# Performance work log

Hardware: AMD Instinct MI355X
Metric: run time of the kernel (lower is better)

## Reference

```python
import jax, jax.numpy as jnp
import numpy as np

EMBED_DIM = 1024
PROJ_DIM = 512
NUM_HEADS = 8
HEAD_DIM = PROJ_DIM // NUM_HEADS
B, L = 2, 2048


def setup_inputs() -> dict:
    key = jax.random.key(0)
    ks = jax.random.split(key, 7)
    s = lambda d: 1.0 / np.sqrt(d)
    return {
        "x": jax.random.normal(ks[0], (B, L, EMBED_DIM), jnp.float32),
        "proj_W": jax.random.normal(ks[1], (EMBED_DIM, PROJ_DIM), jnp.float32) * s(EMBED_DIM),
        "proj_b": jax.random.normal(ks[2], (PROJ_DIM,), jnp.float32) * 0.01,
        "attn_Wq": jax.random.normal(ks[3], (PROJ_DIM, NUM_HEADS, HEAD_DIM), jnp.float32) * s(PROJ_DIM),
        "attn_Wk": jax.random.normal(ks[4], (PROJ_DIM, NUM_HEADS, HEAD_DIM), jnp.float32) * s(PROJ_DIM),
        "attn_Wv": jax.random.normal(ks[5], (PROJ_DIM, NUM_HEADS, HEAD_DIM), jnp.float32) * s(PROJ_DIM),
        "out_W": jax.random.normal(ks[6], (NUM_HEADS * HEAD_DIM, EMBED_DIM), jnp.float32) * s(NUM_HEADS * HEAD_DIM),
    }


def reference(x, proj_W, proj_b, attn_Wq, attn_Wk, attn_Wv, out_W):
    # ReLU projection: (B, L, embed_dim) -> (B, L, proj_dim)
    p = jax.nn.relu(x @ proj_W + proj_b)
    # Per-head projections: (B, L, C) x (C, H, Dh) -> (B, H, L, Dh)
    q = jnp.einsum('blc,chd->bhld', p, attn_Wq)
    k = jnp.einsum('blc,chd->bhld', p, attn_Wk)
    v = jnp.einsum('blc,chd->bhld', p, attn_Wv)
    scale = 1.0 / np.sqrt(HEAD_DIM).astype(np.float32)
    scores = jnp.einsum('bhqd,bhkd->bhqk', q, k) * scale  # (B, H, L, L)
    weights = jax.nn.softmax(scores, axis=-1)
    heads = jnp.einsum('bhqk,bhkd->bhqd', weights, v)  # (B, H, L, Dh)
    heads = heads.transpose(0, 2, 1, 3).reshape(p.shape[0], p.shape[1], NUM_HEADS * HEAD_DIM)
    return heads @ out_W  # (B, L, embed_dim)
```

## Files before the change

### kernel.cpp

```cpp
#include <hip/hip_runtime.h>
#include <math.h>

#define BATCH 2
#define SEQ 2048
#define BL (BATCH * SEQ)
#define EMBED 1024
#define PROJ 512
#define NHEADS 8
#define HDIM 64
#define QKVN (3 * PROJ)
#define KVSPLIT 2
#define KVHALF (SEQ / KVSPLIT)

typedef _Float16 half8 __attribute__((ext_vector_type(8)));
typedef float floatx4 __attribute__((ext_vector_type(4)));

__global__ __launch_bounds__(256) void trconv(const float* __restrict__ src,
                                              _Float16* __restrict__ dst,
                                              int K, int N, float scale) {
    __shared__ float tile[64][65];
    const int t  = threadIdx.x;
    const int n0 = blockIdx.x * 64;
    const int k0 = blockIdx.y * 64;
    const int tx = t & 63;
    const int ty = t >> 6;
#pragma unroll
    for (int i = 0; i < 16; ++i) {
        int k = ty * 16 + i;
        tile[k][tx] = src[(size_t)(k0 + k) * N + n0 + tx];
    }
    __syncthreads();
#pragma unroll
    for (int i = 0; i < 16; ++i) {
        int n = ty * 16 + i;
        dst[(size_t)(n0 + n) * K + k0 + tx] = (_Float16)(tile[tx][n] * scale);
    }
}

__global__ __launch_bounds__(256) void trans_v(const _Float16* __restrict__ v,
                                               _Float16* __restrict__ vt) {
    __shared__ _Float16 tile[64][72];
    const int t  = threadIdx.x;
    const int t0 = blockIdx.x * 64;
    const int h  = blockIdx.y;
    const int b  = blockIdx.z;
    {
        const int r = t >> 2, c0 = (t & 3) * 16;
        const _Float16* src = v + (size_t)(b * SEQ + t0 + r) * QKVN + h * HDIM + c0;
        *reinterpret_cast<half8*>(&tile[r][c0])     = *reinterpret_cast<const half8*>(src);
        *reinterpret_cast<half8*>(&tile[r][c0 + 8]) = *reinterpret_cast<const half8*>(src + 8);
    }
    __syncthreads();
    {
        const int c = t >> 2, k0 = (t & 3) * 16;
        half8 o1, o2;
#pragma unroll
        for (int i = 0; i < 8; ++i) { o1[i] = tile[k0 + i][c]; o2[i] = tile[k0 + 8 + i][c]; }
        _Float16* dst = vt + ((size_t)(b * NHEADS + h) * HDIM + c) * SEQ + t0 + k0;
        *reinterpret_cast<half8*>(dst)     = o1;
        *reinterpret_cast<half8*>(dst + 8) = o2;
    }
}

template <int A_F32, int BIASRELU, int C_F32>
__global__ __launch_bounds__(256) void gemm_mfma(const void* __restrict__ Ap,
                                                 const _Float16* __restrict__ Bt,
                                                 const float* __restrict__ bias,
                                                 void* __restrict__ Cp,
                                                 int M, int N, int K) {
    __shared__ _Float16 Ah[64][40];
    __shared__ _Float16 Bh[64][40];

    const int t  = threadIdx.x;
    const int w  = t >> 6;
    const int l  = t & 63;
    const int lr = l & 15;
    const int lg = l >> 4;
    const int bm = blockIdx.y * 64;
    const int bn = blockIdx.x * 64;
    const int wr = w >> 1;
    const int wc = w & 1;

    const int ar = t >> 2, ac = (t & 3) * 8;

    floatx4 acc[2][2];
#pragma unroll
    for (int i = 0; i < 2; ++i)
#pragma unroll
        for (int j = 0; j < 2; ++j) acc[i][j] = (floatx4){0.f, 0.f, 0.f, 0.f};

    float4 af0, af1;
    half8 areg, breg;

    const float* Af = (const float*)Ap;
    const _Float16* Ah16 = (const _Float16*)Ap;

    if (A_F32) {
        af0 = *reinterpret_cast<const float4*>(&Af[(size_t)(bm + ar) * K + ac]);
        af1 = *reinterpret_cast<const float4*>(&Af[(size_t)(bm + ar) * K + ac + 4]);
    } else {
        areg = *reinterpret_cast<const half8*>(&Ah16[(size_t)(bm + ar) * K + ac]);
    }
    breg = *reinterpret_cast<const half8*>(&Bt[(size_t)(bn + ar) * K + ac]);

    for (int kt = 0; kt < K; kt += 32) {
        if (A_F32) {
            half8 hcv;
            hcv[0] = (_Float16)af0.x; hcv[1] = (_Float16)af0.y;
            hcv[2] = (_Float16)af0.z; hcv[3] = (_Float16)af0.w;
            hcv[4] = (_Float16)af1.x; hcv[5] = (_Float16)af1.y;
            hcv[6] = (_Float16)af1.z; hcv[7] = (_Float16)af1.w;
            *reinterpret_cast<half8*>(&Ah[ar][ac]) = hcv;
        } else {
            *reinterpret_cast<half8*>(&Ah[ar][ac]) = areg;
        }
        *reinterpret_cast<half8*>(&Bh[ar][ac]) = breg;
        __syncthreads();

        if (kt + 32 < K) {
            if (A_F32) {
                af0 = *reinterpret_cast<const float4*>(&Af[(size_t)(bm + ar) * K + kt + 32 + ac]);
                af1 = *reinterpret_cast<const float4*>(&Af[(size_t)(bm + ar) * K + kt + 32 + ac + 4]);
            } else {
                areg = *reinterpret_cast<const half8*>(&Ah16[(size_t)(bm + ar) * K + kt + 32 + ac]);
            }
            breg = *reinterpret_cast<const half8*>(&Bt[(size_t)(bn + ar) * K + kt + 32 + ac]);
        }

        half8 afr[2], bfr[2];
#pragma unroll
        for (int mf = 0; mf < 2; ++mf)
            afr[mf] = *reinterpret_cast<const half8*>(&Ah[wr * 32 + mf * 16 + lr][lg * 8]);
#pragma unroll
        for (int nf = 0; nf < 2; ++nf)
            bfr[nf] = *reinterpret_cast<const half8*>(&Bh[wc * 32 + nf * 16 + lr][lg * 8]);
#pragma unroll
        for (int mf = 0; mf < 2; ++mf)
#pragma unroll
            for (int nf = 0; nf < 2; ++nf)
                acc[mf][nf] = __builtin_amdgcn_mfma_f32_16x16x32_f16(afr[mf], bfr[nf], acc[mf][nf], 0, 0, 0);

        __syncthreads();
    }

#pragma unroll
    for (int mf = 0; mf < 2; ++mf)
#pragma unroll
        for (int nf = 0; nf < 2; ++nf) {
            const int n = bn + wc * 32 + nf * 16 + lr;
            float bs = 0.f;
            if (BIASRELU) bs = bias[n];
#pragma unroll
            for (int r = 0; r < 4; ++r) {
                const int m = bm + wr * 32 + mf * 16 + lg * 4 + r;
                float v = acc[mf][nf][r];
                if (BIASRELU) v = fmaxf(v + bs, 0.f);
                if (C_F32)
                    ((float*)Cp)[(size_t)m * N + n] = v;
                else
                    ((_Float16*)Cp)[(size_t)m * N + n] = (_Float16)v;
            }
        }
}

__global__ __launch_bounds__(256) void attn_part(const _Float16* __restrict__ Q,
                                                 const _Float16* __restrict__ K,
                                                 const _Float16* __restrict__ Vt,
                                                 float* __restrict__ Op,
                                                 float* __restrict__ ml) {
    __shared__ _Float16 Ks[64][72];
    __shared__ _Float16 Vs[64][72];
    __shared__ _Float16 Ps[4][16][72];

    const int t  = threadIdx.x;
    const int w  = t >> 6;
    const int l  = t & 63;
    const int lr = l & 15;
    const int lg = l >> 4;

    const int qt  = blockIdx.x >> 1;
    const int kvh = blockIdx.x & 1;
    const int q0  = qt * 64;
    const int h   = blockIdx.y;
    const int b   = blockIdx.z;
    const size_t base  = (size_t)b * SEQ * QKVN + (size_t)h * HDIM;
    const size_t vbase = (size_t)(b * NHEADS + h) * HDIM * SEQ;
    const size_t poff  = (((size_t)kvh * BATCH + b) * NHEADS + h) * SEQ;

    const int kt0  = kvh * KVHALF;
    const int kend = kt0 + KVHALF;

    half8 qf[2];
#pragma unroll
    for (int s = 0; s < 2; ++s) {
        const int qrow = q0 + w * 16 + lr;
        qf[s] = *reinterpret_cast<const half8*>(
            &Q[base + (size_t)qrow * QKVN + s * 32 + lg * 8]);
    }

    floatx4 o_acc[4];
#pragma unroll
    for (int j = 0; j < 4; ++j) o_acc[j] = (floatx4){0.f, 0.f, 0.f, 0.f};

    float m_s = -1e30f;
    float l_s = 0.f;

    const int rkv = t >> 2;
    const int d0  = (t & 3) * 16;

    half8 ka0, ka1, va0, va1;
    {
        const _Float16* kp = K + base + (size_t)(kt0 + rkv) * QKVN + d0;
        ka0 = *reinterpret_cast<const half8*>(kp);
        ka1 = *reinterpret_cast<const half8*>(kp + 8);
        const _Float16* vp = Vt + vbase + (size_t)rkv * SEQ + kt0 + d0;
        va0 = *reinterpret_cast<const half8*>(vp);
        va1 = *reinterpret_cast<const half8*>(vp + 8);
    }

    for (int kt = kt0; kt < kend; kt += 64) {
        *reinterpret_cast<half8*>(&Ks[rkv][d0])     = ka0;
        *reinterpret_cast<half8*>(&Ks[rkv][d0 + 8]) = ka1;
        *reinterpret_cast<half8*>(&Vs[rkv][d0])     = va0;
        *reinterpret_cast<half8*>(&Vs[rkv][d0 + 8]) = va1;
        __syncthreads();

        if (kt + 64 < kend) {
            const _Float16* kp = K + base + (size_t)(kt + 64 + rkv) * QKVN + d0;
            ka0 = *reinterpret_cast<const half8*>(kp);
            ka1 = *reinterpret_cast<const half8*>(kp + 8);
            const _Float16* vp = Vt + vbase + (size_t)rkv * SEQ + kt + 64 + d0;
            va0 = *reinterpret_cast<const half8*>(vp);
            va1 = *reinterpret_cast<const half8*>(vp + 8);
        }

        floatx4 stv[4];
#pragma unroll
        for (int i = 0; i < 4; ++i) stv[i] = (floatx4){0.f, 0.f, 0.f, 0.f};
#pragma unroll
        for (int s = 0; s < 2; ++s)
#pragma unroll
            for (int mf = 0; mf < 4; ++mf) {
                half8 kfr = *reinterpret_cast<const half8*>(&Ks[mf * 16 + lr][s * 32 + lg * 8]);
                stv[mf] = __builtin_amdgcn_mfma_f32_16x16x32_f16(kfr, qf[s], stv[mf], 0, 0, 0);
            }

        float tm = -1e30f;
#pragma unroll
        for (int mf = 0; mf < 4; ++mf)
#pragma unroll
            for (int r = 0; r < 4; ++r) tm = fmaxf(tm, stv[mf][r]);
        tm = fmaxf(tm, __shfl_xor(tm, 16));
        tm = fmaxf(tm, __shfl_xor(tm, 32));
        float mn = fmaxf(m_s, tm);
        float fscale = exp2f(m_s - mn);
        m_s = mn;
        float sum = 0.f;
#pragma unroll
        for (int mf = 0; mf < 4; ++mf)
#pragma unroll
            for (int r = 0; r < 4; ++r) {
                float p = exp2f(stv[mf][r] - mn);
                stv[mf][r] = p;
                sum += p;
            }
        sum += __shfl_xor(sum, 16);
        sum += __shfl_xor(sum, 32);
        l_s = l_s * fscale + sum;

#pragma unroll
        for (int mf = 0; mf < 4; ++mf)
#pragma unroll
            for (int rp = 0; rp < 2; ++rp) {
                union { _Float16 hh[2]; unsigned int u; } pk;
                pk.hh[0] = (_Float16)stv[mf][2 * rp];
                pk.hh[1] = (_Float16)stv[mf][2 * rp + 1];
                *reinterpret_cast<unsigned int*>(
                    &Ps[w][lr][mf * 16 + lg * 4 + rp * 2]) = pk.u;
            }

#pragma unroll
        for (int r = 0; r < 4; ++r) {
            float f = __shfl(fscale, lg * 4 + r);
#pragma unroll
            for (int nf = 0; nf < 4; ++nf) o_acc[nf][r] *= f;
        }

#pragma unroll
        for (int s = 0; s < 2; ++s) {
            half8 pa = *reinterpret_cast<const half8*>(&Ps[w][lr][s * 32 + lg * 8]);
#pragma unroll
            for (int nf = 0; nf < 4; ++nf) {
                half8 vb = *reinterpret_cast<const half8*>(&Vs[nf * 16 + lr][s * 32 + lg * 8]);
                o_acc[nf] = __builtin_amdgcn_mfma_f32_16x16x32_f16(pa, vb, o_acc[nf], 0, 0, 0);
            }
        }

        __syncthreads();
    }

#pragma unroll
    for (int r = 0; r < 4; ++r) {
        const int qrow = q0 + w * 16 + lg * 4 + r;
#pragma unroll
        for (int nf = 0; nf < 4; ++nf)
            Op[(poff + qrow) * HDIM + nf * 16 + lr] = o_acc[nf][r];
    }
    if (lg == 0) {
        const int qrow = q0 + w * 16 + lr;
        reinterpret_cast<float2*>(ml)[poff + qrow] = make_float2(m_s, l_s);
    }
}

__global__ __launch_bounds__(256) void attn_merge(const float* __restrict__ Op,
                                                  const float* __restrict__ ml,
                                                  _Float16* __restrict__ hd) {
    const int t  = threadIdx.x;
    const int q  = blockIdx.x * 64 + (t >> 2);
    const int d0 = (t & 3) * 16;
    const int h  = blockIdx.y;
    const int b  = blockIdx.z;

    const size_t off0 = ((size_t)b * NHEADS + h) * SEQ + q;
    const size_t off1 = ((size_t)(BATCH + b) * NHEADS + h) * SEQ + q;

    float2 ml0 = reinterpret_cast<const float2*>(ml)[off0];
    float2 ml1 = reinterpret_cast<const float2*>(ml)[off1];
    float m  = fmaxf(ml0.x, ml1.x);
    float a0 = exp2f(ml0.x - m);
    float a1 = exp2f(ml1.x - m);
    float inv = 1.0f / (ml0.y * a0 + ml1.y * a1);
    a0 *= inv; a1 *= inv;

    const float* p0 = Op + off0 * HDIM + d0;
    const float* p1 = Op + off1 * HDIM + d0;
    half8 o[2];
#pragma unroll
    for (int i = 0; i < 4; ++i) {
        float4 v0 = reinterpret_cast<const float4*>(p0)[i];
        float4 v1 = reinterpret_cast<const float4*>(p1)[i];
        o[i >> 1][(i & 1) * 4 + 0] = (_Float16)(v0.x * a0 + v1.x * a1);
        o[i >> 1][(i & 1) * 4 + 1] = (_Float16)(v0.y * a0 + v1.y * a1);
        o[i >> 1][(i & 1) * 4 + 2] = (_Float16)(v0.z * a0 + v1.z * a1);
        o[i >> 1][(i & 1) * 4 + 3] = (_Float16)(v0.w * a0 + v1.w * a1);
    }
    _Float16* dst = hd + (size_t)(b * SEQ + q) * PROJ + h * HDIM + d0;
    *reinterpret_cast<half8*>(dst)     = o[0];
    *reinterpret_cast<half8*>(dst + 8) = o[1];
}

extern "C" void kernel_launch(void* const* d_in, const int* in_sizes, int n_in,
                              void* d_out, int out_size, void* d_ws, size_t ws_size,
                              hipStream_t stream) {
    const float* x  = (const float*)d_in[0];
    const float* pW = (const float*)d_in[1];
    const float* pb = (const float*)d_in[2];
    const float* Wq = (const float*)d_in[3];
    const float* Wk = (const float*)d_in[4];
    const float* Wv = (const float*)d_in[5];
    const float* oW = (const float*)d_in[6];
    float* out = (float*)d_out;

    _Float16* ws    = (_Float16*)d_ws;
    _Float16* p_h   = ws;
    _Float16* qkv   = p_h + (size_t)BL * PROJ;
    _Float16* hd    = qkv + (size_t)BL * QKVN;
    _Float16* pWt   = hd + (size_t)BL * PROJ;
    _Float16* qkvWt = pWt + (size_t)PROJ * EMBED;
    _Float16* oWt   = qkvWt + (size_t)QKVN * PROJ;
    _Float16* vtb   = oWt + (size_t)EMBED * PROJ;
    float*    Opart = (float*)(vtb + (size_t)BATCH * NHEADS * HDIM * SEQ);
    float*    mlb   = Opart + (size_t)KVSPLIT * BATCH * NHEADS * SEQ * HDIM;

    dim3 blk(256);

    trconv<<<dim3(PROJ / 64, EMBED / 64), blk, 0, stream>>>(pW, pWt, EMBED, PROJ, 1.0f);
    trconv<<<dim3(PROJ / 64, PROJ / 64), blk, 0, stream>>>(Wq, qkvWt, PROJ, PROJ, 0.125f * 1.44269504f);
    trconv<<<dim3(PROJ / 64, PROJ / 64), blk, 0, stream>>>(Wk, qkvWt + (size_t)PROJ * PROJ, PROJ, PROJ, 1.0f);
    trconv<<<dim3(PROJ / 64, PROJ / 64), blk, 0, stream>>>(Wv, qkvWt + (size_t)2 * PROJ * PROJ, PROJ, PROJ, 1.0f);
    trconv<<<dim3(EMBED / 64, PROJ / 64), blk, 0, stream>>>(oW, oWt, PROJ, EMBED, 1.0f);

    gemm_mfma<1, 1, 0><<<dim3(PROJ / 64, BL / 64), blk, 0, stream>>>(
        (const void*)x, pWt, pb, (void*)p_h, BL, PROJ, EMBED);

    gemm_mfma<0, 0, 0><<<dim3(QKVN / 64, BL / 64), blk, 0, stream>>>(
        (const void*)p_h, qkvWt, nullptr, (void*)qkv, BL, QKVN, PROJ);

    trans_v<<<dim3(SEQ / 64, NHEADS, BATCH), blk, 0, stream>>>(qkv + 2 * PROJ, vtb);

    attn_part<<<dim3((SEQ / 64) * KVSPLIT, NHEADS, BATCH), blk, 0, stream>>>(
        qkv, qkv + PROJ, vtb, Opart, mlb);
    attn_merge<<<dim3(SEQ / 64, NHEADS, BATCH), blk, 0, stream>>>(Opart, mlb, hd);

    gemm_mfma<0, 0, 1><<<dim3(EMBED / 64, BL / 64), blk, 0, stream>>>(
        (const void*)hd, oWt, nullptr, (void*)out, BL, EMBED, PROJ);
}
```

Before: 122.9 us.

## Templatize GEMM tiles, split KV four ways, lazy rescale, fp16 partials

The GEMM kernel is templated on its block tile, and the QKV and output projections use larger 128-row tiles for more operand reuse. Attention now splits the KV range four ways for more parallelism. Online softmax rescaling is skipped unless the running max grows by more than a threshold, and probabilities are packed to fp16 with cvt_pkrtz. Partial outputs are normalized and stored as fp16 to cut merge traffic, and s_setprio is raised around the MFMA sections. In exchange, the fp16 partials and lazy rescale cost some precision, and the bigger tiles launch fewer blocks.

Result: faster. 115.4 us (-6.2%).

```diff
diff --git a/kernel.cpp b/kernel.cpp
--- a/kernel.cpp
+++ b/kernel.cpp
@@ -9,10 +9,11 @@
 #define NHEADS 8
 #define HDIM 64
 #define QKVN (3 * PROJ)
-#define KVSPLIT 2
-#define KVHALF (SEQ / KVSPLIT)
+#define KVSPLIT 4
+#define KVQ (SEQ / KVSPLIT)
 
 typedef _Float16 half8 __attribute__((ext_vector_type(8)));
+typedef __fp16 fp16x2 __attribute__((ext_vector_type(2)));
 typedef float floatx4 __attribute__((ext_vector_type(4)));
 
 __global__ __launch_bounds__(256) void trconv(const float* __restrict__ src,
@@ -62,97 +63,126 @@
     }
 }
 
-template <int A_F32, int BIASRELU, int C_F32>
+template <int BM, int BN, int A_F32, int BIASRELU, int C_F32>
 __global__ __launch_bounds__(256) void gemm_mfma(const void* __restrict__ Ap,
                                                  const _Float16* __restrict__ Bt,
                                                  const float* __restrict__ bias,
                                                  void* __restrict__ Cp,
                                                  int M, int N, int K) {
-    __shared__ _Float16 Ah[64][40];
-    __shared__ _Float16 Bh[64][40];
+    __shared__ _Float16 Ah[BM][40];
+    __shared__ _Float16 Bh[BN][40];
+
+    constexpr int MF = BM / 32;
+    constexpr int NF = BN / 32;
+    constexpr int EPA = BM / 8;
+    constexpr int TPA = 32 / EPA;
+    constexpr int EPB = BN / 8;
+    constexpr int TPB = 32 / EPB;
 
     const int t  = threadIdx.x;
     const int w  = t >> 6;
     const int l  = t & 63;
     const int lr = l & 15;
     const int lg = l >> 4;
-    const int bm = blockIdx.y * 64;
-    const int bn = blockIdx.x * 64;
+    const int bm = blockIdx.y * BM;
+    const int bn = blockIdx.x * BN;
     const int wr = w >> 1;
     const int wc = w & 1;
 
-    const int ar = t >> 2, ac = (t & 3) * 8;
-
-    floatx4 acc[2][2];
-#pragma unroll
-    for (int i = 0; i < 2; ++i)
-#pragma unroll
-        for (int j = 0; j < 2; ++j) acc[i][j] = (floatx4){0.f, 0.f, 0.f, 0.f};
-
-    float4 af0, af1;
-    half8 areg, breg;
+    const int ar = t / TPA, ac = (t % TPA) * EPA;
+    const int br = t / TPB, bc = (t % TPB) * EPB;
+
+    floatx4 acc[MF][NF];
+#pragma unroll
+    for (int i = 0; i < MF; ++i)
+#pragma unroll
+        for (int j = 0; j < NF; ++j) acc[i][j] = (floatx4){0.f, 0.f, 0.f, 0.f};
+
+    float4 af[EPA / 4];
+    half8  ah[EPA / 8];
+    half8  bh[EPB / 8];
 
     const float* Af = (const float*)Ap;
     const _Float16* Ah16 = (const _Float16*)Ap;
 
     if (A_F32) {
-        af0 = *reinterpret_cast<const float4*>(&Af[(size_t)(bm + ar) * K + ac]);
-        af1 = *reinterpret_cast<const float4*>(&Af[(size_t)(bm + ar) * K + ac + 4]);
+#pragma unroll
+        for (int i = 0; i < EPA / 4; ++i)
+            af[i] = *reinterpret_cast<const float4*>(&Af[(size_t)(bm + ar) * K + ac + i * 4]);
     } else {
-        areg = *reinterpret_cast<const half8*>(&Ah16[(size_t)(bm + ar) * K + ac]);
-    }
-    breg = *reinterpret_cast<const half8*>(&Bt[(size_t)(bn + ar) * K + ac]);
+#pragma unroll
+        for (int i = 0; i < EPA / 8; ++i)
+            ah[i] = *reinterpret_cast<const half8*>(&Ah16[(size_t)(bm + ar) * K + ac + i * 8]);
+    }
+#pragma unroll
+    for (int i = 0; i < EPB / 8; ++i)
+        bh[i] = *reinterpret_cast<const half8*>(&Bt[(size_t)(bn + br) * K + bc + i * 8]);
 
     for (int kt = 0; kt < K; kt += 32) {
         if (A_F32) {
-            half8 hcv;
-            hcv[0] = (_Float16)af0.x; hcv[1] = (_Float16)af0.y;
-            hcv[2] = (_Float16)af0.z; hcv[3] = (_Float16)af0.w;
-            hcv[4] = (_Float16)af1.x; hcv[5] = (_Float16)af1.y;
-            hcv[6] = (_Float16)af1.z; hcv[7] = (_Float16)af1.w;
-            *reinterpret_cast<half8*>(&Ah[ar][ac]) = hcv;
+#pragma unroll
+            for (int i = 0; i < EPA / 8; ++i) {
+                half8 hcv;
+                float4 a0 = af[2 * i], a1 = af[2 * i + 1];
+                hcv[0] = (_Float16)a0.x; hcv[1] = (_Float16)a0.y;
+                hcv[2] = (_Float16)a0.z; hcv[3] = (_Float16)a0.w;
+                hcv[4] = (_Float16)a1.x; hcv[5] = (_Float16)a1.y;
+                hcv[6] = (_Float16)a1.z; hcv[7] = (_Float16)a1.w;
+                *reinterpret_cast<half8*>(&Ah[ar][ac + i * 8]) = hcv;
+            }
         } else {
-            *reinterpret_cast<half8*>(&Ah[ar][ac]) = areg;
-        }
-        *reinterpret_cast<half8*>(&Bh[ar][ac]) = breg;
+#pragma unroll
+            for (int i = 0; i < EPA / 8; ++i)
+                *reinterpret_cast<half8*>(&Ah[ar][ac + i * 8]) = ah[i];
+        }
+#pragma unroll
+        for (int i = 0; i < EPB / 8; ++i)
+            *reinterpret_cast<half8*>(&Bh[br][bc + i * 8]) = bh[i];
         __syncthreads();
 
         if (kt + 32 < K) {
             if (A_F32) {
-                af0 = *reinterpret_cast<const float4*>(&Af[(size_t)(bm + ar) * K + kt + 32 + ac]);
-                af1 = *reinterpret_cast<const float4*>(&Af[(size_t)(bm + ar) * K + kt + 32 + ac + 4]);
+#pragma unroll
+                for (int i = 0; i < EPA / 4; ++i)
+                    af[i] = *reinterpret_cast<const float4*>(&Af[(size_t)(bm + ar) * K + kt + 32 + ac + i * 4]);
             } else {
-                areg = *reinterpret_cast<const half8*>(&Ah16[(size_t)(bm + ar) * K + kt + 32 + ac]);
-            }
-            breg = *reinterpret_cast<const half8*>(&Bt[(size_t)(bn + ar) * K + kt + 32 + ac]);
-        }
-
-        half8 afr[2], bfr[2];
-#pragma unroll
-        for (int mf = 0; mf < 2; ++mf)
-            afr[mf] = *reinterpret_cast<const half8*>(&Ah[wr * 32 + mf * 16 + lr][lg * 8]);
-#pragma unroll
-        for (int nf = 0; nf < 2; ++nf)
-            bfr[nf] = *reinterpret_cast<const half8*>(&Bh[wc * 32 + nf * 16 + lr][lg * 8]);
-#pragma unroll
-        for (int mf = 0; mf < 2; ++mf)
-#pragma unroll
-            for (int nf = 0; nf < 2; ++nf)
+#pragma unroll
+                for (int i = 0; i < EPA / 8; ++i)
+                    ah[i] = *reinterpret_cast<const half8*>(&Ah16[(size_t)(bm + ar) * K + kt + 32 + ac + i * 8]);
+            }
+#pragma unroll
+            for (int i = 0; i < EPB / 8; ++i)
+                bh[i] = *reinterpret_cast<const half8*>(&Bt[(size_t)(bn + br) * K + kt + 32 + bc + i * 8]);
+        }
+
+        half8 afr[MF], bfr[NF];
+#pragma unroll
+        for (int mf = 0; mf < MF; ++mf)
+            afr[mf] = *reinterpret_cast<const half8*>(&Ah[wr * (BM / 2) + mf * 16 + lr][lg * 8]);
+#pragma unroll
+        for (int nf = 0; nf < NF; ++nf)
+            bfr[nf] = *reinterpret_cast<const half8*>(&Bh[wc * (BN / 2) + nf * 16 + lr][lg * 8]);
+        __builtin_amdgcn_s_setprio(1);
+#pragma unroll
+        for (int mf = 0; mf < MF; ++mf)
+#pragma unroll
+            for (int nf = 0; nf < NF; ++nf)
                 acc[mf][nf] = __builtin_amdgcn_mfma_f32_16x16x32_f16(afr[mf], bfr[nf], acc[mf][nf], 0, 0, 0);
+        __builtin_amdgcn_s_setprio(0);
 
         __syncthreads();
     }
 
 #pragma unroll
-    for (int mf = 0; mf < 2; ++mf)
-#pragma unroll
-        for (int nf = 0; nf < 2; ++nf) {
-            const int n = bn + wc * 32 + nf * 16 + lr;
+    for (int mf = 0; mf < MF; ++mf)
+#pragma unroll
+        for (int nf = 0; nf < NF; ++nf) {
+            const int n = bn + wc * (BN / 2) + nf * 16 + lr;
             float bs = 0.f;
             if (BIASRELU) bs = bias[n];
 #pragma unroll
             for (int r = 0; r < 4; ++r) {
-                const int m = bm + wr * 32 + mf * 16 + lg * 4 + r;
+                const int m = bm + wr * (BM / 2) + mf * 16 + lg * 4 + r;
                 float v = acc[mf][nf][r];
                 if (BIASRELU) v = fmaxf(v + bs, 0.f);
                 if (C_F32)
@@ -166,7 +196,7 @@
 __global__ __launch_bounds__(256) void attn_part(const _Float16* __restrict__ Q,
                                                  const _Float16* __restrict__ K,
                                                  const _Float16* __restrict__ Vt,
-                                                 float* __restrict__ Op,
+                                                 _Float16* __restrict__ Op,
                                                  float* __restrict__ ml) {
     __shared__ _Float16 Ks[64][72];
     __shared__ _Float16 Vs[64][72];
@@ -178,17 +208,17 @@
     const int lr = l & 15;
     const int lg = l >> 4;
 
-    const int qt  = blockIdx.x >> 1;
-    const int kvh = blockIdx.x & 1;
+    const int qt  = blockIdx.x >> 2;
+    const int kvs = blockIdx.x & 3;
     const int q0  = qt * 64;
     const int h   = blockIdx.y;
     const int b   = blockIdx.z;
     const size_t base  = (size_t)b * SEQ * QKVN + (size_t)h * HDIM;
     const size_t vbase = (size_t)(b * NHEADS + h) * HDIM * SEQ;
-    const size_t poff  = (((size_t)kvh * BATCH + b) * NHEADS + h) * SEQ;
-
-    const int kt0  = kvh * KVHALF;
-    const int kend = kt0 + KVHALF;
+    const size_t poff  = (((size_t)kvs * BATCH + b) * NHEADS + h) * SEQ;
+
+    const int kt0  = kvs * KVQ;
+    const int kend = kt0 + KVQ;
 
     half8 qf[2];
 #pragma unroll
@@ -237,6 +267,7 @@
         floatx4 stv[4];
 #pragma unroll
         for (int i = 0; i < 4; ++i) stv[i] = (floatx4){0.f, 0.f, 0.f, 0.f};
+        __builtin_amdgcn_s_setprio(1);
 #pragma unroll
         for (int s = 0; s < 2; ++s)
 #pragma unroll
@@ -244,6 +275,7 @@
                 half8 kfr = *reinterpret_cast<const half8*>(&Ks[mf * 16 + lr][s * 32 + lg * 8]);
                 stv[mf] = __builtin_amdgcn_mfma_f32_16x16x32_f16(kfr, qf[s], stv[mf], 0, 0, 0);
             }
+        __builtin_amdgcn_s_setprio(0);
 
         float tm = -1e30f;
 #pragma unroll
@@ -252,40 +284,40 @@
             for (int r = 0; r < 4; ++r) tm = fmaxf(tm, stv[mf][r]);
         tm = fmaxf(tm, __shfl_xor(tm, 16));
         tm = fmaxf(tm, __shfl_xor(tm, 32));
-        float mn = fmaxf(m_s, tm);
-        float fscale = exp2f(m_s - mn);
-        m_s = mn;
+        if (!__all(tm <= m_s + 8.f)) {
+            float mn = fmaxf(m_s, tm);
+            float fs = exp2f(m_s - mn);
+            m_s = mn;
+            l_s *= fs;
+#pragma unroll
+            for (int r = 0; r < 4; ++r) {
+                float f = __shfl(fs, lg * 4 + r);
+#pragma unroll
+                for (int nf = 0; nf < 4; ++nf) o_acc[nf][r] *= f;
+            }
+        }
         float sum = 0.f;
 #pragma unroll
         for (int mf = 0; mf < 4; ++mf)
 #pragma unroll
             for (int r = 0; r < 4; ++r) {
-                float p = exp2f(stv[mf][r] - mn);
+                float p = exp2f(stv[mf][r] - m_s);
                 stv[mf][r] = p;
                 sum += p;
             }
         sum += __shfl_xor(sum, 16);
         sum += __shfl_xor(sum, 32);
-        l_s = l_s * fscale + sum;
-
-#pragma unroll
-        for (int mf = 0; mf < 4; ++mf)
-#pragma unroll
-            for (int rp = 0; rp < 2; ++rp) {
-                union { _Float16 hh[2]; unsigned int u; } pk;
-                pk.hh[0] = (_Float16)stv[mf][2 * rp];
-                pk.hh[1] = (_Float16)stv[mf][2 * rp + 1];
-                *reinterpret_cast<unsigned int*>(
-                    &Ps[w][lr][mf * 16 + lg * 4 + rp * 2]) = pk.u;
-            }
-
-#pragma unroll
-        for (int r = 0; r < 4; ++r) {
-            float f = __shfl(fscale, lg * 4 + r);
-#pragma unroll
-            for (int nf = 0; nf < 4; ++nf) o_acc[nf][r] *= f;
-        }
-
+        l_s += sum;
+
+#pragma unroll
+        for (int mf = 0; mf < 4; ++mf) {
+            fp16x2 pk0 = __builtin_amdgcn_cvt_pkrtz(stv[mf][0], stv[mf][1]);
+            fp16x2 pk1 = __builtin_amdgcn_cvt_pkrtz(stv[mf][2], stv[mf][3]);
+            *reinterpret_cast<fp16x2*>(&Ps[w][lr][mf * 16 + lg * 4])     = pk0;
+            *reinterpret_cast<fp16x2*>(&Ps[w][lr][mf * 16 + lg * 4 + 2]) = pk1;
+        }
+
+        __builtin_amdgcn_s_setprio(1);
 #pragma unroll
         for (int s = 0; s < 2; ++s) {
             half8 pa = *reinterpret_cast<const half8*>(&Ps[w][lr][s * 32 + lg * 8]);
@@ -295,6 +327,7 @@
                 o_acc[nf] = __builtin_amdgcn_mfma_f32_16x16x32_f16(pa, vb, o_acc[nf], 0, 0, 0);
             }
         }
+        __builtin_amdgcn_s_setprio(0);
 
         __syncthreads();
     }
@@ -302,9 +335,10 @@
 #pragma unroll
     for (int r = 0; r < 4; ++r) {
         const int qrow = q0 + w * 16 + lg * 4 + r;
+        float inv = 1.0f / __shfl(l_s, lg * 4 + r);
 #pragma unroll
         for (int nf = 0; nf < 4; ++nf)
-            Op[(poff + qrow) * HDIM + nf * 16 + lr] = o_acc[nf][r];
+            Op[(poff + qrow) * HDIM + nf * 16 + lr] = (_Float16)(o_acc[nf][r] * inv);
     }
     if (lg == 0) {
         const int qrow = q0 + w * 16 + lr;
@@ -312,7 +346,7 @@
     }
 }
 
-__global__ __launch_bounds__(256) void attn_merge(const float* __restrict__ Op,
+__global__ __launch_bounds__(256) void attn_merge(const _Float16* __restrict__ Op,
                                                   const float* __restrict__ ml,
                                                   _Float16* __restrict__ hd) {
     const int t  = threadIdx.x;
@@ -321,32 +355,44 @@
     const int h  = blockIdx.y;
     const int b  = blockIdx.z;
 
-    const size_t off0 = ((size_t)b * NHEADS + h) * SEQ + q;
-    const size_t off1 = ((size_t)(BATCH + b) * NHEADS + h) * SEQ + q;
-
-    float2 ml0 = reinterpret_cast<const float2*>(ml)[off0];
-    float2 ml1 = reinterpret_cast<const float2*>(ml)[off1];
-    float m  = fmaxf(ml0.x, ml1.x);
-    float a0 = exp2f(ml0.x - m);
-    float a1 = exp2f(ml1.x - m);
-    float inv = 1.0f / (ml0.y * a0 + ml1.y * a1);
-    a0 *= inv; a1 *= inv;
-
-    const float* p0 = Op + off0 * HDIM + d0;
-    const float* p1 = Op + off1 * HDIM + d0;
-    half8 o[2];
-#pragma unroll
-    for (int i = 0; i < 4; ++i) {
-        float4 v0 = reinterpret_cast<const float4*>(p0)[i];
-        float4 v1 = reinterpret_cast<const float4*>(p1)[i];
-        o[i >> 1][(i & 1) * 4 + 0] = (_Float16)(v0.x * a0 + v1.x * a1);
-        o[i >> 1][(i & 1) * 4 + 1] = (_Float16)(v0.y * a0 + v1.y * a1);
-        o[i >> 1][(i & 1) * 4 + 2] = (_Float16)(v0.z * a0 + v1.z * a1);
-        o[i >> 1][(i & 1) * 4 + 3] = (_Float16)(v0.w * a0 + v1.w * a1);
-    }
+    size_t offs[KVSPLIT];
+    float2 mls[KVSPLIT];
+#pragma unroll
+    for (int s = 0; s < KVSPLIT; ++s) {
+        offs[s] = (((size_t)s * BATCH + b) * NHEADS + h) * SEQ + q;
+        mls[s] = reinterpret_cast<const float2*>(ml)[offs[s]];
+    }
+    float m = mls[0].x;
+#pragma unroll
+    for (int s = 1; s < KVSPLIT; ++s) m = fmaxf(m, mls[s].x);
+    float wgt[KVSPLIT];
+    float wsum = 0.f;
+#pragma unroll
+    for (int s = 0; s < KVSPLIT; ++s) {
+        wgt[s] = mls[s].y * exp2f(mls[s].x - m);
+        wsum += wgt[s];
+    }
+    float inv = 1.0f / wsum;
+
+    float o[16] = {};
+#pragma unroll
+    for (int s = 0; s < KVSPLIT; ++s) {
+        const _Float16* p = Op + offs[s] * HDIM + d0;
+        half8 a = *reinterpret_cast<const half8*>(p);
+        half8 c = *reinterpret_cast<const half8*>(p + 8);
+        float wv = wgt[s] * inv;
+#pragma unroll
+        for (int i = 0; i < 8; ++i) {
+            o[i]     += wv * (float)a[i];
+            o[8 + i] += wv * (float)c[i];
+        }
+    }
+    half8 o0, o1;
+#pragma unroll
+    for (int i = 0; i < 8; ++i) { o0[i] = (_Float16)o[i]; o1[i] = (_Float16)o[8 + i]; }
     _Float16* dst = hd + (size_t)(b * SEQ + q) * PROJ + h * HDIM + d0;
-    *reinterpret_cast<half8*>(dst)     = o[0];
-    *reinterpret_cast<half8*>(dst + 8) = o[1];
+    *reinterpret_cast<half8*>(dst)     = o0;
+    *reinterpret_cast<half8*>(dst + 8) = o1;
 }
 
 extern "C" void kernel_launch(void* const* d_in, const int* in_sizes, int n_in,
@@ -369,8 +415,8 @@
     _Float16* qkvWt = pWt + (size_t)PROJ * EMBED;
     _Float16* oWt   = qkvWt + (size_t)QKVN * PROJ;
     _Float16* vtb   = oWt + (size_t)EMBED * PROJ;
-    float*    Opart = (float*)(vtb + (size_t)BATCH * NHEADS * HDIM * SEQ);
-    float*    mlb   = Opart + (size_t)KVSPLIT * BATCH * NHEADS * SEQ * HDIM;
+    _Float16* Oph   = vtb + (size_t)BATCH * NHEADS * HDIM * SEQ;
+    float*    mlb   = (float*)(Oph + (size_t)KVSPLIT * BATCH * NHEADS * SEQ * HDIM);
 
     dim3 blk(256);
 
@@ -380,18 +426,18 @@
     trconv<<<dim3(PROJ / 64, PROJ / 64), blk, 0, stream>>>(Wv, qkvWt + (size_t)2 * PROJ * PROJ, PROJ, PROJ, 1.0f);
     trconv<<<dim3(EMBED / 64, PROJ / 64), blk, 0, stream>>>(oW, oWt, PROJ, EMBED, 1.0f);
 
-    gemm_mfma<1, 1, 0><<<dim3(PROJ / 64, BL / 64), blk, 0, stream>>>(
+    gemm_mfma<64, 64, 1, 1, 0><<<dim3(PROJ / 64, BL / 64), blk, 0, stream>>>(
         (const void*)x, pWt, pb, (void*)p_h, BL, PROJ, EMBED);
 
-    gemm_mfma<0, 0, 0><<<dim3(QKVN / 64, BL / 64), blk, 0, stream>>>(
+    gemm_mfma<128, 128, 0, 0, 0><<<dim3(QKVN / 128, BL / 128), blk, 0, stream>>>(
         (const void*)p_h, qkvWt, nullptr, (void*)qkv, BL, QKVN, PROJ);
 
     trans_v<<<dim3(SEQ / 64, NHEADS, BATCH), blk, 0, stream>>>(qkv + 2 * PROJ, vtb);
 
     attn_part<<<dim3((SEQ / 64) * KVSPLIT, NHEADS, BATCH), blk, 0, stream>>>(
-        qkv, qkv + PROJ, vtb, Opart, mlb);
-    attn_merge<<<dim3(SEQ / 64, NHEADS, BATCH), blk, 0, stream>>>(Opart, mlb, hd);
-
-    gemm_mfma<0, 0, 1><<<dim3(EMBED / 64, BL / 64), blk, 0, stream>>>(
+        qkv, qkv + PROJ, vtb, Oph, mlb);
+    attn_merge<<<dim3(SEQ / 64, NHEADS, BATCH), blk, 0, stream>>>(Oph, mlb, hd);
+
+    gemm_mfma<128, 64, 0, 0, 1><<<dim3(EMBED / 64, BL / 128), blk, 0, stream>>>(
         (const void*)hd, oWt, nullptr, (void*)out, BL, EMBED, PROJ);
 }
```
